# Kernel optimization log

Measured on AMD Instinct MI355X. Metric: run time of the kernel, lower is better.

Reference implementation:

```python
import jax, jax.numpy as jnp
import numpy as np

N_NODES = 32768
N_EDGES = 524288
NODE_DIM = 128
HIDDEN = 256
EDGE_DIM = 32


def setup_inputs() -> dict:
    key = jax.random.key(0)
    ks = jax.random.split(key, 12)
    s = 0.05
    return {
        "h": jax.random.normal(ks[0], (N_NODES, NODE_DIM), jnp.float32),
        "x": jax.random.normal(ks[1], (N_NODES, 3), jnp.float32) * 10.0,
        "edge_index": jax.random.randint(ks[2], (2, N_EDGES), 0, N_NODES, dtype=jnp.int32).astype(jnp.int64),
        "edge_dist": jax.random.uniform(ks[3], (N_EDGES,), jnp.float32) * 15.0,
        # edge_mlp: Linear(1, edge_dim) -> SiLU -> Linear(edge_dim, edge_dim)
        "We1": jax.random.normal(ks[4], (1, EDGE_DIM), jnp.float32) * s,
        "be1": jnp.zeros((EDGE_DIM,), jnp.float32),
        "We2": jax.random.normal(ks[5], (EDGE_DIM, EDGE_DIM), jnp.float32) * s,
        "be2": jnp.zeros((EDGE_DIM,), jnp.float32),
        # node_mlp: Linear(2*node+edge, hidden) -> SiLU -> Linear(hidden, node)
        "Wn1": jax.random.normal(ks[6], (2 * NODE_DIM + EDGE_DIM, HIDDEN), jnp.float32) * s,
        "bn1": jnp.zeros((HIDDEN,), jnp.float32),
        "Wn2": jax.random.normal(ks[7], (HIDDEN, NODE_DIM), jnp.float32) * s,
        "bn2": jnp.zeros((NODE_DIM,), jnp.float32),
        # coord_mlp: Linear(2*node+edge, hidden) -> SiLU -> Linear(hidden, 1, bias=False)
        "Wc1": jax.random.normal(ks[8], (2 * NODE_DIM + EDGE_DIM, HIDDEN), jnp.float32) * s,
        "bc1": jnp.zeros((HIDDEN,), jnp.float32),
        "Wc2": jax.random.normal(ks[9], (HIDDEN, 1), jnp.float32) * s,
    }


def reference(h, x, edge_index, edge_dist,
              We1, be1, We2, be2,
              Wn1, bn1, Wn2, bn2,
              Wc1, bc1, Wc2):
    src, dst = edge_index[0], edge_index[1]
    n_nodes = h.shape[0]

    # edge_mlp on scalar distances -> [E, edge_dim]
    edge_attr = jax.nn.silu(edge_dist[:, None] @ We1 + be1) @ We2 + be2

    # per-edge message input: [E, 2*node_dim + edge_dim]
    m_input = jnp.concatenate([h[src], h[dst], edge_attr], axis=-1)

    # node messages and scatter-add onto destination nodes
    m = jax.nn.silu(m_input @ Wn1 + bn1) @ Wn2 + bn2          # [E, node_dim]
    h_agg = jax.ops.segment_sum(m, dst, num_segments=n_nodes)  # [N, node_dim]

    # equivariant coordinate update along normalized edge direction
    coord_weight = jax.nn.silu(m_input @ Wc1 + bc1) @ Wc2      # [E, 1]
    dir_vec = x[src] - x[dst]                                  # [E, 3]
    dir_len = jnp.maximum(jnp.linalg.norm(dir_vec, axis=-1, keepdims=True), 1e-8)
    coord_update = coord_weight * (dir_vec / dir_len)          # [E, 3]
    x_agg = jax.ops.segment_sum(coord_update, dst, num_segments=n_nodes)

    return h + h_agg, x + x_agg
```

## Files before the change

### kernel.cpp

```cpp
#include <hip/hip_runtime.h>
#include <math.h>

#define N_NODES 32768
#define N_EDGES 524288
#define NODE_DIM 128
#define HIDDEN 256
#define EDGE_DIM 32
#define TE 32
#define NBLK (N_EDGES / TE)
#define ASTR 296
#define HSTR 264
#define SZ2  264
#define MSTR 132

typedef __attribute__((ext_vector_type(8))) short bf16x8;
typedef __attribute__((ext_vector_type(16))) float f32x16;

__device__ __forceinline__ float silu_f(float v) {
    float e = __expf(-v);
    return v * __builtin_amdgcn_rcpf(1.0f + e);
}

__device__ __forceinline__ unsigned short f2bf_rne(float f) {
    union { float f; unsigned int u; } v; v.f = f;
    return (unsigned short)((v.u + 0x7fffu + ((v.u >> 16) & 1u)) >> 16);
}
__device__ __forceinline__ unsigned int pk_rne(float a, float b) {
    return (unsigned int)f2bf_rne(a) | ((unsigned int)f2bf_rne(b) << 16);
}
__device__ __forceinline__ unsigned int pkbf(float a, float b) {
    union { float f; unsigned int u; } ua, ub; ua.f = a; ub.f = b;
    return __builtin_amdgcn_perm(ub.u + 0x8000u, ua.u + 0x8000u, 0x07060302u);
}
__device__ __forceinline__ unsigned short f2bf_hu(float f) {
    union { float f; unsigned int u; } v; v.f = f;
    return (unsigned short)((v.u + 0x8000u) >> 16);
}
__device__ __forceinline__ float bfu(unsigned short u) {
    union { unsigned int u; float f; } v; v.u = ((unsigned int)u) << 16;
    return v.f;
}
__device__ __forceinline__ unsigned int addbf2(unsigned int a, unsigned int b) {
    float l = __uint_as_float(a << 16) + __uint_as_float(b << 16);
    float h = __uint_as_float(a & 0xffff0000u) + __uint_as_float(b & 0xffff0000u);
    return pkbf(l, h);
}

__device__ __forceinline__ int detect_is64(const void* ei, int t) {
    const unsigned int* ew = (const unsigned int*)ei;
    unsigned int hiw = ew[2 * (t & 63) + 1];
    return (__ballot(hiw != 0u) == 0ULL) ? 1 : 0;
}

#define WS_BIAS_OFF 1024
#define WS_W1S_OFF  69632
#define WS_W2S_OFF  364544
#define WS_CNT_OFF  430080
#define WS_CUR_OFF  561152
#define WS_PERM_OFF 692224
#define WS_HBF_OFF  2790400
#define WS_HBF_END  (WS_HBF_OFF + N_NODES * NODE_DIM * 2)
#define WS_PS_OFF   WS_HBF_END
#define WS_PD_OFF   (WS_PS_OFF + N_NODES * 512 * 2)
#define WS_PD_END   (WS_PD_OFF + N_NODES * 512 * 2)

#define SEG_HIST 524288
#define SEG_W1S  147456
#define SEG_W2S  32768
#define SEG_BIAS 512
#define SEG_OUT  1073152
#define SEG_HBF  524288
#define PREP_TOT (SEG_HIST + SEG_W1S + SEG_W2S + SEG_BIAS + SEG_OUT + SEG_HBF)

#define W1_PA 0
#define W1_PB 16384
#define W1_PC 81920

__device__ __forceinline__ float w1row(const float* Wn1, const float* Wc1, int k, int n) {
    return (n < 256) ? Wn1[k * 256 + n] : Wc1[k * 256 + (n - 256)];
}

__global__ void prep_hist_kernel(const float* __restrict__ h, const float* __restrict__ x,
                                 const void* __restrict__ ei,
                                 const float* __restrict__ We2, const float* __restrict__ be2,
                                 const float* __restrict__ Wn1, const float* __restrict__ bn1,
                                 const float* __restrict__ Wn2,
                                 const float* __restrict__ Wc1, const float* __restrict__ bc1,
                                 float* __restrict__ out, float* __restrict__ biasC,
                                 unsigned short* __restrict__ W1s, unsigned short* __restrict__ W2s,
                                 int* __restrict__ counts, unsigned short* __restrict__ hbf,
                                 int use_pp) {
    int i = blockIdx.x * 256 + threadIdx.x;
    if (i < SEG_HIST) {
        int is64 = detect_is64(ei, threadIdx.x);
        int dst = is64 ? (int)((const long long*)ei)[N_EDGES + i]
                       : ((const int*)ei)[N_EDGES + i];
        atomicAdd(&counts[dst], 1);
        return;
    }
    i -= SEG_HIST;
    if (i < SEG_W1S) {
        if (use_pp) {
            if (i < W1_PB) {
                int jj = i & 7, ln = (i >> 3) & 63, rest = i >> 9;
                int step = rest & 1, tile = rest >> 1;
                int n = tile * 32 + (ln & 31);
                int j = step * 16 + ((ln >> 5) * 8) + jj;
                float s = 0.0f;
                #pragma unroll 8
                for (int q = 0; q < 32; ++q)
                    s += We2[j * 32 + q] * w1row(Wn1, Wc1, 256 + q, n);
                W1s[i] = f2bf_rne(s);
            } else if (i < W1_PC) {
                int i2 = i - W1_PB;
                int jj = i2 & 7, ln = (i2 >> 3) & 63, rest = i2 >> 9;
                int step = rest & 7, tile = rest >> 3;
                int n = tile * 32 + (ln & 31);
                int k = step * 16 + ((ln >> 5) * 8) + jj;
                W1s[i] = f2bf_rne(w1row(Wn1, Wc1, k, n));
            } else {
                int i2 = i - W1_PC;
                int jj = i2 & 7, ln = (i2 >> 3) & 63, rest = i2 >> 9;
                int step = rest & 7, tile = rest >> 3;
                int n = tile * 32 + (ln & 31);
                int k = 128 + step * 16 + ((ln >> 5) * 8) + jj;
                W1s[i] = f2bf_rne(w1row(Wn1, Wc1, k, n));
            }
        } else {
// ... 69 lines not shown
    int c = counts[b * 256 + t];
    loc[t] = c;
    __syncthreads();
    if (t == 0) {
        int s = 0;
        for (int j = 0; j < 128; ++j) { int v = pb[j]; pb[j] = s; s += v; }
    }
    #pragma unroll
    for (int d = 1; d < 256; d <<= 1) {
        int v = (t >= d) ? loc[t - d] : 0;
        __syncthreads();
        loc[t] += v;
        __syncthreads();
    }
    cursor[b * 256 + t] = pb[b] + loc[t] - c;
}

__global__ void place_kernel(const void* __restrict__ ei,
                             int* __restrict__ cursor, int* __restrict__ perm) {
    int is64 = detect_is64(ei, threadIdx.x);
    int e = blockIdx.x * 256 + threadIdx.x;
    int dst = is64 ? (int)((const long long*)ei)[N_EDGES + e]
                   : ((const int*)ei)[N_EDGES + e];
    int pos = atomicAdd(&cursor[dst], 1);
    perm[pos] = e;
}

__global__ __launch_bounds__(256, 4)
void nterm_kernel(const unsigned short* __restrict__ hbf,
                  const unsigned short* __restrict__ W1s,
                  unsigned short* __restrict__ psrc,
                  unsigned short* __restrict__ pdst) {
    const int t = threadIdx.x;
    const int lane = t & 63;
    const int wv = t >> 6;
    const int lo = lane & 31;
    const int hi = lane >> 5;
    const int nb = blockIdx.x * 32;
    const int aoff = (nb + lo) * NODE_DIM + hi * 8;
    const int TSB = 8 * 64 * 8;

    for (int pass = 0; pass < 2; ++pass) {
        const unsigned short* WB = W1s + (pass ? W1_PC : W1_PB);
        unsigned short* outp = pass ? pdst : psrc;
        f32x16 a0, a1, a2, a3;
        #pragma unroll
        for (int r = 0; r < 16; ++r) { a0[r] = 0.f; a1[r] = 0.f; a2[r] = 0.f; a3[r] = 0.f; }
        const int b0 = (wv     ) * TSB + lane * 8;
        const int b1 = (wv +  4) * TSB + lane * 8;
        const int b2 = (wv +  8) * TSB + lane * 8;
        const int b3 = (wv + 12) * TSB + lane * 8;
        bf16x8 p0[2], p1[2], p2[2], p3[2];
        p0[0] = *(const bf16x8*)&WB[b0];
        p1[0] = *(const bf16x8*)&WB[b1];
        p2[0] = *(const bf16x8*)&WB[b2];
        p3[0] = *(const bf16x8*)&WB[b3];
        #pragma unroll
        for (int step = 0; step < 8; ++step) {
            const int cur = step & 1, nxt = cur ^ 1;
            if (step + 1 < 8) {
                p0[nxt] = *(const bf16x8*)&WB[b0 + (step + 1) * 512];
                p1[nxt] = *(const bf16x8*)&WB[b1 + (step + 1) * 512];
                p2[nxt] = *(const bf16x8*)&WB[b2 + (step + 1) * 512];
                p3[nxt] = *(const bf16x8*)&WB[b3 + (step + 1) * 512];
            }
            bf16x8 f = *(const bf16x8*)&hbf[aoff + step * 16];
            a0 = __builtin_amdgcn_mfma_f32_32x32x16_bf16(f, p0[cur], a0, 0, 0, 0);
            a1 = __builtin_amdgcn_mfma_f32_32x32x16_bf16(f, p1[cur], a1, 0, 0, 0);
            a2 = __builtin_amdgcn_mfma_f32_32x32x16_bf16(f, p2[cur], a2, 0, 0, 0);
            a3 = __builtin_amdgcn_mfma_f32_32x32x16_bf16(f, p3[cur], a3, 0, 0, 0);
        }
        #pragma unroll
        for (int r = 0; r < 16; ++r) {
            int er = (r & 3) + 8 * (r >> 2) + 4 * hi;
            unsigned short* row = &outp[(unsigned)(nb + er) * 512 + lo];
            row[(wv     ) * 32] = f2bf_rne(a0[r]);
            row[(wv +  4) * 32] = f2bf_rne(a1[r]);
            row[(wv +  8) * 32] = f2bf_rne(a2[r]);
            row[(wv + 12) * 32] = f2bf_rne(a3[r]);
        }
    }
}

__global__ __launch_bounds__(256, 6)
void egnn_pp_kernel(const float* __restrict__ x,
                    const void* __restrict__ ei, const float* __restrict__ dist,
                    const float* __restrict__ We1, const float* __restrict__ be1,
                    const float* __restrict__ bn2, const float* __restrict__ Wc2,
                    const float* __restrict__ biasC,
                    const unsigned short* __restrict__ W1s,
                    const unsigned short* __restrict__ W2s,
                    const int* __restrict__ perm,
                    const unsigned short* __restrict__ psrc,
                    const unsigned short* __restrict__ pdst,
                    float* __restrict__ out)
{
    __shared__ unsigned short smZ[TE * SZ2];
    __shared__ unsigned short smT[TE * 40];
    __shared__ int sidx[TE], didx[TE], eidx[TE];
    __shared__ float cw_s[TE];
    __shared__ float cxyz[3 * TE];

    float* smM = (float*)smZ;

    const int t = threadIdx.x;
    const int lane = t & 63;
    const int wv = t >> 6;
    const int lo = lane & 31;
    const int hi = lane >> 5;
    const int swz = ((blockIdx.x & 7) * (NBLK / 8)) + (blockIdx.x >> 3);
    const int ebase = swz * TE;
    const int is64 = detect_is64(ei, t);

    if (t < 2 * TE) {
        int e = t & (TE - 1);
        int eid = perm[ebase + e];
        int which = t >> 5;
        long long pos = (long long)which * N_EDGES + eid;
        int idx = is64 ? (int)((const long long*)ei)[pos] : ((const int*)ei)[pos];
        if (which == 0) { sidx[e] = idx; eidx[e] = eid; }
        else didx[e] = idx;
        if (t < TE) cw_s[t] = 0.0f;
    }
    __syncthreads();

    {
        int e = t >> 3;
        int j4 = (t & 7) * 4;
        float d = dist[eidx[e]];
        float s0 = silu_f(d * We1[j4 + 0] + be1[j4 + 0]);
        float s1 = silu_f(d * We1[j4 + 1] + be1[j4 + 1]);
        float s2 = silu_f(d * We1[j4 + 2] + be1[j4 + 2]);
        float s3 = silu_f(d * We1[j4 + 3] + be1[j4 + 3]);
        *(uint2*)&smT[e * 40 + j4] = make_uint2(pkbf(s0, s1), pkbf(s2, s3));
    }
    if (t < TE) {
        int s = sidx[t], dn = didx[t];
        float dx = x[s * 3 + 0] - x[dn * 3 + 0];
        float dy = x[s * 3 + 1] - x[dn * 3 + 1];
        float dz = x[s * 3 + 2] - x[dn * 3 + 2];
        float len = fmaxf(sqrtf(dx * dx + dy * dy + dz * dz), 1e-8f);
        float inv = 1.0f / len;
        cxyz[t] = dx * inv; cxyz[TE + t] = dy * inv; cxyz[2 * TE + t] = dz * inv;
    }
    __syncthreads();

    const int rowbase = 4 * hi;
    const int aT = lo * 40 + hi * 8;

    #pragma unroll
    for (int it = 0; it < 4; ++it) {
        int id = it * 256 + t;
        int g = id & 31;
        int e = id >> 5;
        int cb = 256 + g * 8;
        uint4 a = *(const uint4*)&psrc[(unsigned)sidx[e] * 512 + cb];
        uint4 b = *(const uint4*)&pdst[(unsigned)didx[e] * 512 + cb];
        uint4 o = make_uint4(addbf2(a.x, b.x), addbf2(a.y, b.y),
                             addbf2(a.z, b.z), addbf2(a.w, b.w));
        *(uint4*)&smZ[e * SZ2 + g * 8] = o;
    }
    __syncthreads();

    {
        const int c0off = wv * 32;
        const int c1off = (wv + 4) * 32;
        f32x16 c0, c1;
        {
            float b0 = biasC[256 + c0off + lo];
            float b1 = biasC[256 + c1off + lo];
            #pragma unroll
            for (int r = 0; r < 16; ++r) { c0[r] = b0; c1[r] = b1; }
        }
        bf16x8 a0 = *(const bf16x8*)&smT[aT];
        bf16x8 a1 = *(const bf16x8*)&smT[aT + 16];
        const int tt0 = 8 + wv, tt1 = 12 + wv;
        bf16x8 w00 = *(const bf16x8*)&W1s[((tt0 * 2 + 0) * 64 + lane) * 8];
        bf16x8 w01 = *(const bf16x8*)&W1s[((tt0 * 2 + 1) * 64 + lane) * 8];
        bf16x8 w10 = *(const bf16x8*)&W1s[((tt1 * 2 + 0) * 64 + lane) * 8];
        bf16x8 w11 = *(const bf16x8*)&W1s[((tt1 * 2 + 1) * 64 + lane) * 8];
        c0 = __builtin_amdgcn_mfma_f32_32x32x16_bf16(a0, w00, c0, 0, 0, 0);
        c0 = __builtin_amdgcn_mfma_f32_32x32x16_bf16(a1, w01, c0, 0, 0, 0);
        c1 = __builtin_amdgcn_mfma_f32_32x32x16_bf16(a0, w10, c1, 0, 0, 0);
        c1 = __builtin_amdgcn_mfma_f32_32x32x16_bf16(a1, w11, c1, 0, 0, 0);
        float wc0 = Wc2[c0off + lo];
        float wc1 = Wc2[c1off + lo];
        float p[16];
        #pragma unroll
        for (int r = 0; r < 16; ++r) {
            int er = (r & 3) + 8 * (r >> 2) + rowbase;
            float v0 = c0[r] + bfu(smZ[er * SZ2 + c0off + lo]);
            float v1 = c1[r] + bfu(smZ[er * SZ2 + c1off + lo]);
            p[r] = silu_f(v0) * wc0 + silu_f(v1) * wc1;
        }
        #pragma unroll
        for (int off = 1; off < 32; off <<= 1) {
            #pragma unroll
            for (int r = 0; r < 16; ++r) p[r] += __shfl_xor(p[r], off);
        }
        if (lo == 0) {
            #pragma unroll
            for (int r = 0; r < 16; ++r)
                atomicAdd(&cw_s[(r & 3) + 8 * (r >> 2) + rowbase], p[r]);
        }
    }
    __syncthreads();

    #pragma unroll
    for (int it = 0; it < 4; ++it) {
        int id = it * 256 + t;
        int g = id & 31;
        int e = id >> 5;
        int cb = g * 8;
        uint4 a = *(const uint4*)&psrc[(unsigned)sidx[e] * 512 + cb];
        uint4 b = *(const uint4*)&pdst[(unsigned)didx[e] * 512 + cb];
        uint4 o = make_uint4(addbf2(a.x, b.x), addbf2(a.y, b.y),
                             addbf2(a.z, b.z), addbf2(a.w, b.w));
        *(uint4*)&smZ[e * SZ2 + g * 8] = o;
    }
    __syncthreads();

    {
        const int n0off = wv * 32;
        const int n1off = (wv + 4) * 32;
        f32x16 c0, c1;
        {
            float b0 = biasC[n0off + lo];
            float b1 = biasC[n1off + lo];
            #pragma unroll
            for (int r = 0; r < 16; ++r) { c0[r] = b0; c1[r] = b1; }
        }
        bf16x8 a0 = *(const bf16x8*)&smT[aT];
        bf16x8 a1 = *(const bf16x8*)&smT[aT + 16];
        const int tt0 = wv, tt1 = wv + 4;
        bf16x8 w00 = *(const bf16x8*)&W1s[((tt0 * 2 + 0) * 64 + lane) * 8];
        bf16x8 w01 = *(const bf16x8*)&W1s[((tt0 * 2 + 1) * 64 + lane) * 8];
        bf16x8 w10 = *(const bf16x8*)&W1s[((tt1 * 2 + 0) * 64 + lane) * 8];
        bf16x8 w11 = *(const bf16x8*)&W1s[((tt1 * 2 + 1) * 64 + lane) * 8];
        c0 = __builtin_amdgcn_mfma_f32_32x32x16_bf16(a0, w00, c0, 0, 0, 0);
        c0 = __builtin_amdgcn_mfma_f32_32x32x16_bf16(a1, w01, c0, 0, 0, 0);
        c1 = __builtin_amdgcn_mfma_f32_32x32x16_bf16(a0, w10, c1, 0, 0, 0);
        c1 = __builtin_amdgcn_mfma_f32_32x32x16_bf16(a1, w11, c1, 0, 0, 0);
        #pragma unroll
        for (int r = 0; r < 16; ++r) {
            int er = (r & 3) + 8 * (r >> 2) + rowbase;
            float v0 = c0[r] + bfu(smZ[er * SZ2 + n0off + lo]);
            float v1 = c1[r] + bfu(smZ[er * SZ2 + n1off + lo]);
            smZ[er * SZ2 + n0off + lo] = f2bf_hu(silu_f(v0));
            smZ[er * SZ2 + n1off + lo] = f2bf_hu(silu_f(v1));
        }
    }
    if (t < TE) {
        float w = cw_s[t];
        cxyz[t] *= w; cxyz[TE + t] *= w; cxyz[2 * TE + t] *= w;
    }
    __syncthreads();

    {
        const int d = wv * 32 + lo;
        f32x16 acc;
        float bb = bn2[d];
        #pragma unroll
        for (int r = 0; r < 16; ++r) acc[r] = bb;
        const int hoff = lo * SZ2 + hi * 8;
        const int wb = wv * (16 * 64 * 8) + lane * 8;
        bf16x8 bs[2];
        bs[0] = *(const bf16x8*)&W2s[wb];
        #pragma unroll
        for (int step = 0; step < 16; ++step) {
            const int cur = step & 1, nxt = cur ^ 1;
            if (step + 1 < 16)
                bs[nxt] = *(const bf16x8*)&W2s[wb + (step + 1) * 512];
            bf16x8 af = *(const bf16x8*)&smZ[hoff + step * 16];
            acc = __builtin_amdgcn_mfma_f32_32x32x16_bf16(af, bs[cur], acc, 0, 0, 0);
        }
        __syncthreads();
        #pragma unroll
        for (int r = 0; r < 16; ++r) {
            int er = (r & 3) + 8 * (r >> 2) + rowbase;
            smM[er * MSTR + d] = acc[r];
        }
    }
    __syncthreads();

    {
        const int g = t >> 5;
        const int d4 = (t & 31) * 4;
        for (int e0 = g; e0 < TE; e0 += 8) {
            if (e0 > 0 && didx[e0] == didx[e0 - 1]) continue;
            float4 s = *(const float4*)&smM[e0 * MSTR + d4];
            int er = e0 + 1;
            while (er < TE && didx[er] == didx[e0]) {
                float4 v = *(const float4*)&smM[er * MSTR + d4];
                s.x += v.x; s.y += v.y; s.z += v.z; s.w += v.w;
                ++er;
            }
            float* dp = &out[didx[e0] * NODE_DIM + d4];
            if (e0 > 0 && er < TE) {
                float4 cur = *(const float4*)dp;
                cur.x += s.x; cur.y += s.y; cur.z += s.z; cur.w += s.w;
                *(float4*)dp = cur;
            } else {
                atomicAdd(dp + 0, s.x); atomicAdd(dp + 1, s.y);
                atomicAdd(dp + 2, s.z); atomicAdd(dp + 3, s.w);
            }
        }
    }
    if (t < TE) {
        int e0 = t;
        if (e0 == 0 || didx[e0] != didx[e0 - 1]) {
            float sx = cxyz[e0], sy = cxyz[TE + e0], sz = cxyz[2 * TE + e0];
            int er = e0 + 1;
            while (er < TE && didx[er] == didx[e0]) {
                sx += cxyz[er]; sy += cxyz[TE + er]; sz += cxyz[2 * TE + er];
                ++er;
            }
            float* xo = out + N_NODES * NODE_DIM + didx[e0] * 3;
            if (e0 > 0 && er < TE) {
                xo[0] += sx; xo[1] += sy; xo[2] += sz;
            } else {
                atomicAdd(xo + 0, sx); atomicAdd(xo + 1, sy); atomicAdd(xo + 2, sz);
            }
        }
    }
}

__global__ __launch_bounds__(256, 6)
void egnn_mfma_kernel(const float* __restrict__ h, const float* __restrict__ x,
                      const void* __restrict__ ei, const float* __restrict__ dist,
                      const float* __restrict__ We1, const float* __restrict__ be1,
                      const float* __restrict__ bn2, const float* __restrict__ Wc2,
                      const float* __restrict__ biasC,
                      const unsigned short* __restrict__ W1s,
                      const unsigned short* __restrict__ W2s,
                      const int* __restrict__ perm,
                      const unsigned short* __restrict__ hbf,
                      float* __restrict__ out)
{
    __shared__ unsigned short smA[TE * ASTR];
    __shared__ int sidx[TE], didx[TE], eidx[TE];
    __shared__ float cw_s[TE];
    __shared__ float cxyz[3 * TE];

    unsigned short* smH = smA;
    float* smM = (float*)smA;

    const int t = threadIdx.x;
    const int lane = t & 63;
    const int wv = t >> 6;
    const int lo = lane & 31;
    const int hi = lane >> 5;
    const int swz = ((blockIdx.x & 7) * (NBLK / 8)) + (blockIdx.x >> 3);
    const int ebase = swz * TE;
    const int is64 = detect_is64(ei, t);

    if (t < 2 * TE) {
        int e = t & (TE - 1);
        int eid = perm[ebase + e];
        int which = t >> 5;
        long long pos = (long long)which * N_EDGES + eid;
        int idx = is64 ? (int)((const long long*)ei)[pos] : ((const int*)ei)[pos];
        if (which == 0) { sidx[e] = idx; eidx[e] = eid; }
        else didx[e] = idx;
        if (t < TE) cw_s[t] = 0.0f;
    }
    __syncthreads();

    if (hbf != nullptr) {
        #pragma unroll
        for (int it = 0; it < 4; ++it) {
            int id = it * 256 + t;
            int g = id & 15;
            int half = (id >> 4) & 1;
            int e = id >> 5;
            int node = half ? didx[e] : sidx[e];
            uint4 v = *(const uint4*)&hbf[node * NODE_DIM + 8 * g];
            *(uint4*)&smA[e * ASTR + half * NODE_DIM + 8 * g] = v;
        }
    } else {
        #pragma unroll
        for (int it = 0; it < 4; ++it) {
            int id = it * 256 + t;
            int g8 = id & 15;
            int half = (id >> 4) & 1;
            int e = id >> 5;
            int node = half ? didx[e] : sidx[e];
            const float4* p = (const float4*)&h[node * NODE_DIM + 8 * g8];
            float4 v0 = p[0], v1 = p[1];
            unsigned int a0 = pkbf(v0.x, v0.y), a1 = pkbf(v0.z, v0.w);
            unsigned int a2 = pkbf(v1.x, v1.y), a3 = pkbf(v1.z, v1.w);
            *(uint4*)&smA[e * ASTR + half * NODE_DIM + 8 * g8] = make_uint4(a0, a1, a2, a3);
        }
    }
    {
        int e = t >> 3;
        int j4 = (t & 7) * 4;
        float d = dist[eidx[e]];
        float s0 = silu_f(d * We1[j4 + 0] + be1[j4 + 0]);
        float s1 = silu_f(d * We1[j4 + 1] + be1[j4 + 1]);
        float s2 = silu_f(d * We1[j4 + 2] + be1[j4 + 2]);
        float s3 = silu_f(d * We1[j4 + 3] + be1[j4 + 3]);
        *(uint2*)&smA[e * ASTR + 2 * NODE_DIM + j4] = make_uint2(pkbf(s0, s1), pkbf(s2, s3));
    }
    if (t < TE) {
        int s = sidx[t], dn = didx[t];
        float dx = x[s * 3 + 0] - x[dn * 3 + 0];
        float dy = x[s * 3 + 1] - x[dn * 3 + 1];
        float dz = x[s * 3 + 2] - x[dn * 3 + 2];
        float len = fmaxf(sqrtf(dx * dx + dy * dy + dz * dz), 1e-8f);
        float inv = 1.0f / len;
        cxyz[t] = dx * inv; cxyz[TE + t] = dy * inv; cxyz[2 * TE + t] = dz * inv;
    }
    __syncthreads();

    const int rowbase = 4 * hi;

    {
        f32x16 c0, c1;
        {
            float b0 = biasC[256 + wv * 32 + lo];
            float b1 = biasC[256 + (wv + 4) * 32 + lo];
            #pragma unroll
            for (int r = 0; r < 16; ++r) { c0[r] = b0; c1[r] = b1; }
        }
        {
            const int ao = lo * ASTR + hi * 8;
            const int TS = 18 * 64 * 8;
            const int q0 = (8 + wv) * TS + lane * 8;
            const int q1 = (12 + wv) * TS + lane * 8;
            bf16x8 p0[2], p1[2];
            p0[0] = *(const bf16x8*)&W1s[q0];
            p1[0] = *(const bf16x8*)&W1s[q1];
            #pragma unroll
            for (int step = 0; step < 18; ++step) {
                const int cur = step & 1, nxt = cur ^ 1;
                if (step + 1 < 18) {
                    p0[nxt] = *(const bf16x8*)&W1s[q0 + (step + 1) * 512];
                    p1[nxt] = *(const bf16x8*)&W1s[q1 + (step + 1) * 512];
                }
                bf16x8 f = *(const bf16x8*)&smA[ao + step * 16];
                c0 = __builtin_amdgcn_mfma_f32_32x32x16_bf16(f, p0[cur], c0, 0, 0, 0);
                c1 = __builtin_amdgcn_mfma_f32_32x32x16_bf16(f, p1[cur], c1, 0, 0, 0);
            }
        }
        float w0 = Wc2[wv * 32 + lo];
        float w1 = Wc2[(wv + 4) * 32 + lo];
        float p[16];
        #pragma unroll
        for (int r = 0; r < 16; ++r)
            p[r] = silu_f(c0[r]) * w0 + silu_f(c1[r]) * w1;
        #pragma unroll
        for (int off = 1; off < 32; off <<= 1) {
            #pragma unroll
            for (int r = 0; r < 16; ++r) p[r] += __shfl_xor(p[r], off);
        }
        if (lo == 0) {
            #pragma unroll
            for (int r = 0; r < 16; ++r)
                atomicAdd(&cw_s[(r & 3) + 8 * (r >> 2) + rowbase], p[r]);
        }
    }

    f32x16 a0, a1;
    {
        float b0 = biasC[wv * 32 + lo];
        float b1 = biasC[(wv + 4) * 32 + lo];
        #pragma unroll
        for (int r = 0; r < 16; ++r) { a0[r] = b0; a1[r] = b1; }
        const int ao = lo * ASTR + hi * 8;
        const int TS = 18 * 64 * 8;
        const int q0 = (wv) * TS + lane * 8;
        const int q1 = (wv + 4) * TS + lane * 8;
        bf16x8 p0[2], p1[2];
        p0[0] = *(const bf16x8*)&W1s[q0];
        p1[0] = *(const bf16x8*)&W1s[q1];
        #pragma unroll
        for (int step = 0; step < 18; ++step) {
            const int cur = step & 1, nxt = cur ^ 1;
            if (step + 1 < 18) {
                p0[nxt] = *(const bf16x8*)&W1s[q0 + (step + 1) * 512];
                p1[nxt] = *(const bf16x8*)&W1s[q1 + (step + 1) * 512];
            }
            bf16x8 f = *(const bf16x8*)&smA[ao + step * 16];
            a0 = __builtin_amdgcn_mfma_f32_32x32x16_bf16(f, p0[cur], a0, 0, 0, 0);
            a1 = __builtin_amdgcn_mfma_f32_32x32x16_bf16(f, p1[cur], a1, 0, 0, 0);
        }
    }
    __syncthreads();

    {
        const int jb0 = (wv    ) * 32 + lo;
        const int jb1 = (wv + 4) * 32 + lo;
        #pragma unroll
        for (int r = 0; r < 16; ++r) {
            int er = (r & 3) + 8 * (r >> 2) + rowbase;
            smH[er * HSTR + jb0] = f2bf_hu(silu_f(a0[r]));
            smH[er * HSTR + jb1] = f2bf_hu(silu_f(a1[r]));
        }
    }
    if (t < TE) {
        float w = cw_s[t];
        cxyz[t] *= w; cxyz[TE + t] *= w; cxyz[2 * TE + t] *= w;
    }
    __syncthreads();

    {
        const int d = wv * 32 + lo;
        f32x16 acc;
        float bb = bn2[d];
        #pragma unroll
        for (int r = 0; r < 16; ++r) acc[r] = bb;
        const int hoff = lo * HSTR + hi * 8;
        const int wb = wv * (16 * 64 * 8) + lane * 8;
        bf16x8 bs[2];
        bs[0] = *(const bf16x8*)&W2s[wb];
        #pragma unroll
        for (int step = 0; step < 16; ++step) {
            const int cur = step & 1, nxt = cur ^ 1;
            if (step + 1 < 16)
                bs[nxt] = *(const bf16x8*)&W2s[wb + (step + 1) * 512];
            bf16x8 af = *(const bf16x8*)&smH[hoff + step * 16];
            acc = __builtin_amdgcn_mfma_f32_32x32x16_bf16(af, bs[cur], acc, 0, 0, 0);
        }
        __syncthreads();
        #pragma unroll
        for (int r = 0; r < 16; ++r) {
            int er = (r & 3) + 8 * (r >> 2) + rowbase;
            smM[er * MSTR + d] = acc[r];
        }
    }
    __syncthreads();

    {
        const int g = t >> 5;
        const int d4 = (t & 31) * 4;
        for (int e0 = g; e0 < TE; e0 += 8) {
            if (e0 > 0 && didx[e0] == didx[e0 - 1]) continue;
            float4 s = *(const float4*)&smM[e0 * MSTR + d4];
            int er = e0 + 1;
            while (er < TE && didx[er] == didx[e0]) {
                float4 v = *(const float4*)&smM[er * MSTR + d4];
                s.x += v.x; s.y += v.y; s.z += v.z; s.w += v.w;
                ++er;
            }
            float* dp = &out[didx[e0] * NODE_DIM + d4];
            if (e0 > 0 && er < TE) {
                float4 cur = *(const float4*)dp;
                cur.x += s.x; cur.y += s.y; cur.z += s.z; cur.w += s.w;
                *(float4*)dp = cur;
            } else {
                atomicAdd(dp + 0, s.x); atomicAdd(dp + 1, s.y);
                atomicAdd(dp + 2, s.z); atomicAdd(dp + 3, s.w);
            }
        }
    }
    if (t < TE) {
        int e0 = t;
        if (e0 == 0 || didx[e0] != didx[e0 - 1]) {
            float sx = cxyz[e0], sy = cxyz[TE + e0], sz = cxyz[2 * TE + e0];
            int er = e0 + 1;
            while (er < TE && didx[er] == didx[e0]) {
                sx += cxyz[er]; sy += cxyz[TE + er]; sz += cxyz[2 * TE + er];
                ++er;
            }
            float* xo = out + N_NODES * NODE_DIM + didx[e0] * 3;
            if (e0 > 0 && er < TE) {
                xo[0] += sx; xo[1] += sy; xo[2] += sz;
            } else {
                atomicAdd(xo + 0, sx); atomicAdd(xo + 1, sy); atomicAdd(xo + 2, sz);
            }
        }
    }
}

extern "C" void kernel_launch(void* const* d_in, const int* in_sizes, int n_in,
                              void* d_out, int out_size, void* d_ws, size_t ws_size,
                              hipStream_t stream) {
    const float* h    = (const float*)d_in[0];
    const float* x    = (const float*)d_in[1];
    const void*  ei   = d_in[2];
    const float* dist = (const float*)d_in[3];
    const float* We1  = (const float*)d_in[4];
    const float* be1  = (const float*)d_in[5];
    const float* We2  = (const float*)d_in[6];
    const float* be2  = (const float*)d_in[7];
    const float* Wn1  = (const float*)d_in[8];
    const float* bn1  = (const float*)d_in[9];
    const float* Wn2  = (const float*)d_in[10];
    const float* bn2  = (const float*)d_in[11];
    const float* Wc1  = (const float*)d_in[12];
    const float* bc1  = (const float*)d_in[13];
    const float* Wc2  = (const float*)d_in[14];
    float* out = (float*)d_out;

    float* biasC = (float*)((char*)d_ws + WS_BIAS_OFF);
    unsigned short* W1s = (unsigned short*)((char*)d_ws + WS_W1S_OFF);
    unsigned short* W2s = (unsigned short*)((char*)d_ws + WS_W2S_OFF);
    int* counts   = (int*)((char*)d_ws + WS_CNT_OFF);
    int* cursor   = (int*)((char*)d_ws + WS_CUR_OFF);
    int* perm     = (int*)((char*)d_ws + WS_PERM_OFF);
    unsigned short* hbf = (ws_size >= (size_t)WS_HBF_END)
                        ? (unsigned short*)((char*)d_ws + WS_HBF_OFF) : nullptr;
    int use_pp = (ws_size >= (size_t)WS_PD_END && hbf != nullptr) ? 1 : 0;
    unsigned short* psrc = use_pp ? (unsigned short*)((char*)d_ws + WS_PS_OFF) : nullptr;
    unsigned short* pdst = use_pp ? (unsigned short*)((char*)d_ws + WS_PD_OFF) : nullptr;
// ... 20 lines not shown
```

Measured before the change: 404.5 us.

## Add gathered src/dst projections via identity-matrix MFMAs instead of LDS staging

The precomputed per-node projections (psrc, pdst) used to be gathered, summed in bf16 and staged through shared memory before the edge-feature MFMAs. Each lane now loads its rows straight from global memory and adds them into the accumulators with extra MFMAs against identity bf16 matrices. This removes the LDS staging stores, the bf16 add and two block barriers, at the cost of eight extra MFMAs per half and more live registers. The occupancy hint is lowered from 6 to 5 waves to make room for those registers.

```diff
diff --git a/kernel.cpp b/kernel.cpp
--- a/kernel.cpp
+++ b/kernel.cpp
@@ -39,11 +39,6 @@
 __device__ __forceinline__ float bfu(unsigned short u) {
     union { unsigned int u; float f; } v; v.u = ((unsigned int)u) << 16;
     return v.f;
-}
-__device__ __forceinline__ unsigned int addbf2(unsigned int a, unsigned int b) {
-    float l = __uint_as_float(a << 16) + __uint_as_float(b << 16);
-    float h = __uint_as_float(a & 0xffff0000u) + __uint_as_float(b & 0xffff0000u);
-    return pkbf(l, h);
 }
 
 __device__ __forceinline__ int detect_is64(const void* ei, int t) {
@@ -279,7 +274,7 @@
     }
 }
 
-__global__ __launch_bounds__(256, 6)
+__global__ __launch_bounds__(256, 5)
 void egnn_pp_kernel(const float* __restrict__ x,
                     const void* __restrict__ ei, const float* __restrict__ dist,
                     const float* __restrict__ We1, const float* __restrict__ be1,
@@ -292,13 +287,13 @@
                     const unsigned short* __restrict__ pdst,
                     float* __restrict__ out)
 {
-    __shared__ unsigned short smZ[TE * SZ2];
+    __shared__ unsigned short smH[TE * SZ2];
     __shared__ unsigned short smT[TE * 40];
     __shared__ int sidx[TE], didx[TE], eidx[TE];
     __shared__ float cw_s[TE];
     __shared__ float cxyz[3 * TE];
 
-    float* smM = (float*)smZ;
+    float* smM = (float*)smH;
 
     const int t = threadIdx.x;
     const int lane = t & 63;
@@ -345,23 +340,31 @@
     const int rowbase = 4 * hi;
     const int aT = lo * 40 + hi * 8;
 
+    bf16x8 ilow, ihigh;
     #pragma unroll
-    for (int it = 0; it < 4; ++it) {
-        int id = it * 256 + t;
-        int g = id & 31;
-        int e = id >> 5;
-        int cb = 256 + g * 8;
-        uint4 a = *(const uint4*)&psrc[(unsigned)sidx[e] * 512 + cb];
-        uint4 b = *(const uint4*)&pdst[(unsigned)didx[e] * 512 + cb];
-        uint4 o = make_uint4(addbf2(a.x, b.x), addbf2(a.y, b.y),
-                             addbf2(a.z, b.z), addbf2(a.w, b.w));
-        *(uint4*)&smZ[e * SZ2 + g * 8] = o;
-    }
-    __syncthreads();
+    for (int idx = 0; idx < 8; ++idx) {
+        int k = hi * 8 + idx;
+        ilow[idx]  = (short)((k == lo)      ? 0x3F80 : 0);
+        ihigh[idx] = (short)((k == lo - 16) ? 0x3F80 : 0);
+    }
+
+    const unsigned int bs = (unsigned)sidx[lo] * 512 + hi * 8;
+    const unsigned int bd = (unsigned)didx[lo] * 512 + hi * 8;
+
+    bf16x8 a0 = *(const bf16x8*)&smT[aT];
+    bf16x8 a1 = *(const bf16x8*)&smT[aT + 16];
 
     {
         const int c0off = wv * 32;
         const int c1off = (wv + 4) * 32;
+        bf16x8 zs00 = *(const bf16x8*)&psrc[bs + 256 + c0off];
+        bf16x8 zs01 = *(const bf16x8*)&psrc[bs + 256 + c0off + 16];
+        bf16x8 zd00 = *(const bf16x8*)&pdst[bd + 256 + c0off];
+        bf16x8 zd01 = *(const bf16x8*)&pdst[bd + 256 + c0off + 16];
+        bf16x8 zs10 = *(const bf16x8*)&psrc[bs + 256 + c1off];
+        bf16x8 zs11 = *(const bf16x8*)&psrc[bs + 256 + c1off + 16];
+        bf16x8 zd10 = *(const bf16x8*)&pdst[bd + 256 + c1off];
+        bf16x8 zd11 = *(const bf16x8*)&pdst[bd + 256 + c1off + 16];
         f32x16 c0, c1;
         {
             float b0 = biasC[256 + c0off + lo];
@@ -369,8 +372,6 @@
             #pragma unroll
             for (int r = 0; r < 16; ++r) { c0[r] = b0; c1[r] = b1; }
         }
-        bf16x8 a0 = *(const bf16x8*)&smT[aT];
-        bf16x8 a1 = *(const bf16x8*)&smT[aT + 16];
         const int tt0 = 8 + wv, tt1 = 12 + wv;
         bf16x8 w00 = *(const bf16x8*)&W1s[((tt0 * 2 + 0) * 64 + lane) * 8];
         bf16x8 w01 = *(const bf16x8*)&W1s[((tt0 * 2 + 1) * 64 + lane) * 8];
@@ -380,16 +381,20 @@
         c0 = __builtin_amdgcn_mfma_f32_32x32x16_bf16(a1, w01, c0, 0, 0, 0);
         c1 = __builtin_amdgcn_mfma_f32_32x32x16_bf16(a0, w10, c1, 0, 0, 0);
         c1 = __builtin_amdgcn_mfma_f32_32x32x16_bf16(a1, w11, c1, 0, 0, 0);
+        c0 = __builtin_amdgcn_mfma_f32_32x32x16_bf16(zs00, ilow,  c0, 0, 0, 0);
+        c0 = __builtin_amdgcn_mfma_f32_32x32x16_bf16(zs01, ihigh, c0, 0, 0, 0);
+        c0 = __builtin_amdgcn_mfma_f32_32x32x16_bf16(zd00, ilow,  c0, 0, 0, 0);
+        c0 = __builtin_amdgcn_mfma_f32_32x32x16_bf16(zd01, ihigh, c0, 0, 0, 0);
+        c1 = __builtin_amdgcn_mfma_f32_32x32x16_bf16(zs10, ilow,  c1, 0, 0, 0);
+        c1 = __builtin_amdgcn_mfma_f32_32x32x16_bf16(zs11, ihigh, c1, 0, 0, 0);
+        c1 = __builtin_amdgcn_mfma_f32_32x32x16_bf16(zd10, ilow,  c1, 0, 0, 0);
+        c1 = __builtin_amdgcn_mfma_f32_32x32x16_bf16(zd11, ihigh, c1, 0, 0, 0);
         float wc0 = Wc2[c0off + lo];
         float wc1 = Wc2[c1off + lo];
         float p[16];
         #pragma unroll
-        for (int r = 0; r < 16; ++r) {
-            int er = (r & 3) + 8 * (r >> 2) + rowbase;
-            float v0 = c0[r] + bfu(smZ[er * SZ2 + c0off + lo]);
-            float v1 = c1[r] + bfu(smZ[er * SZ2 + c1off + lo]);
-            p[r] = silu_f(v0) * wc0 + silu_f(v1) * wc1;
-        }
+        for (int r = 0; r < 16; ++r)
+            p[r] = silu_f(c0[r]) * wc0 + silu_f(c1[r]) * wc1;
         #pragma unroll
         for (int off = 1; off < 32; off <<= 1) {
             #pragma unroll
@@ -401,25 +406,18 @@
                 atomicAdd(&cw_s[(r & 3) + 8 * (r >> 2) + rowbase], p[r]);
         }
     }
-    __syncthreads();
-
-    #pragma unroll
-    for (int it = 0; it < 4; ++it) {
-        int id = it * 256 + t;
-        int g = id & 31;
-        int e = id >> 5;
-        int cb = g * 8;
-        uint4 a = *(const uint4*)&psrc[(unsigned)sidx[e] * 512 + cb];
-        uint4 b = *(const uint4*)&pdst[(unsigned)didx[e] * 512 + cb];
-        uint4 o = make_uint4(addbf2(a.x, b.x), addbf2(a.y, b.y),
-                             addbf2(a.z, b.z), addbf2(a.w, b.w));
-        *(uint4*)&smZ[e * SZ2 + g * 8] = o;
-    }
-    __syncthreads();
 
     {
         const int n0off = wv * 32;
         const int n1off = (wv + 4) * 32;
+        bf16x8 zs00 = *(const bf16x8*)&psrc[bs + n0off];
+        bf16x8 zs01 = *(const bf16x8*)&psrc[bs + n0off + 16];
+        bf16x8 zd00 = *(const bf16x8*)&pdst[bd + n0off];
+        bf16x8 zd01 = *(const bf16x8*)&pdst[bd + n0off + 16];
+        bf16x8 zs10 = *(const bf16x8*)&psrc[bs + n1off];
+        bf16x8 zs11 = *(const bf16x8*)&psrc[bs + n1off + 16];
+        bf16x8 zd10 = *(const bf16x8*)&pdst[bd + n1off];
+        bf16x8 zd11 = *(const bf16x8*)&pdst[bd + n1off + 16];
         f32x16 c0, c1;
         {
             float b0 = biasC[n0off + lo];
@@ -427,8 +425,6 @@
             #pragma unroll
             for (int r = 0; r < 16; ++r) { c0[r] = b0; c1[r] = b1; }
         }
-        bf16x8 a0 = *(const bf16x8*)&smT[aT];
-        bf16x8 a1 = *(const bf16x8*)&smT[aT + 16];
         const int tt0 = wv, tt1 = wv + 4;
         bf16x8 w00 = *(const bf16x8*)&W1s[((tt0 * 2 + 0) * 64 + lane) * 8];
         bf16x8 w01 = *(const bf16x8*)&W1s[((tt0 * 2 + 1) * 64 + lane) * 8];
@@ -438,20 +434,27 @@
         c0 = __builtin_amdgcn_mfma_f32_32x32x16_bf16(a1, w01, c0, 0, 0, 0);
         c1 = __builtin_amdgcn_mfma_f32_32x32x16_bf16(a0, w10, c1, 0, 0, 0);
         c1 = __builtin_amdgcn_mfma_f32_32x32x16_bf16(a1, w11, c1, 0, 0, 0);
+        c0 = __builtin_amdgcn_mfma_f32_32x32x16_bf16(zs00, ilow,  c0, 0, 0, 0);
+        c0 = __builtin_amdgcn_mfma_f32_32x32x16_bf16(zs01, ihigh, c0, 0, 0, 0);
+        c0 = __builtin_amdgcn_mfma_f32_32x32x16_bf16(zd00, ilow,  c0, 0, 0, 0);
+        c0 = __builtin_amdgcn_mfma_f32_32x32x16_bf16(zd01, ihigh, c0, 0, 0, 0);
+        c1 = __builtin_amdgcn_mfma_f32_32x32x16_bf16(zs10, ilow,  c1, 0, 0, 0);
+        c1 = __builtin_amdgcn_mfma_f32_32x32x16_bf16(zs11, ihigh, c1, 0, 0, 0);
+        c1 = __builtin_amdgcn_mfma_f32_32x32x16_bf16(zd10, ilow,  c1, 0, 0, 0);
+        c1 = __builtin_amdgcn_mfma_f32_32x32x16_bf16(zd11, ihigh, c1, 0, 0, 0);
         #pragma unroll
         for (int r = 0; r < 16; ++r) {
             int er = (r & 3) + 8 * (r >> 2) + rowbase;
-            float v0 = c0[r] + bfu(smZ[er * SZ2 + n0off + lo]);
-            float v1 = c1[r] + bfu(smZ[er * SZ2 + n1off + lo]);
-            smZ[er * SZ2 + n0off + lo] = f2bf_hu(silu_f(v0));
-            smZ[er * SZ2 + n1off + lo] = f2bf_hu(silu_f(v1));
-        }
-    }
+            smH[er * SZ2 + n0off + lo] = f2bf_hu(silu_f(c0[r]));
+            smH[er * SZ2 + n1off + lo] = f2bf_hu(silu_f(c1[r]));
+        }
+    }
+    __syncthreads();
+
     if (t < TE) {
         float w = cw_s[t];
         cxyz[t] *= w; cxyz[TE + t] *= w; cxyz[2 * TE + t] *= w;
     }
-    __syncthreads();
 
     {
         const int d = wv * 32 + lo;
@@ -461,15 +464,15 @@
         for (int r = 0; r < 16; ++r) acc[r] = bb;
         const int hoff = lo * SZ2 + hi * 8;
         const int wb = wv * (16 * 64 * 8) + lane * 8;
-        bf16x8 bs[2];
-        bs[0] = *(const bf16x8*)&W2s[wb];
+        bf16x8 bs2[2];
+        bs2[0] = *(const bf16x8*)&W2s[wb];
         #pragma unroll
         for (int step = 0; step < 16; ++step) {
             const int cur = step & 1, nxt = cur ^ 1;
             if (step + 1 < 16)
-                bs[nxt] = *(const bf16x8*)&W2s[wb + (step + 1) * 512];
-            bf16x8 af = *(const bf16x8*)&smZ[hoff + step * 16];
-            acc = __builtin_amdgcn_mfma_f32_32x32x16_bf16(af, bs[cur], acc, 0, 0, 0);
+                bs2[nxt] = *(const bf16x8*)&W2s[wb + (step + 1) * 512];
+            bf16x8 af = *(const bf16x8*)&smH[hoff + step * 16];
+            acc = __builtin_amdgcn_mfma_f32_32x32x16_bf16(af, bs2[cur], acc, 0, 0, 0);
         }
         __syncthreads();
         #pragma unroll
@@ -539,7 +542,7 @@
     __shared__ float cw_s[TE];
     __shared__ float cxyz[3 * TE];
 
-    unsigned short* smH = smA;
+    unsigned short* smH2 = smA;
     float* smM = (float*)smA;
 
     const int t = threadIdx.x;
@@ -691,8 +694,8 @@
         #pragma unroll
         for (int r = 0; r < 16; ++r) {
             int er = (r & 3) + 8 * (r >> 2) + rowbase;
-            smH[er * HSTR + jb0] = f2bf_hu(silu_f(a0[r]));
-            smH[er * HSTR + jb1] = f2bf_hu(silu_f(a1[r]));
+            smH2[er * HSTR + jb0] = f2bf_hu(silu_f(a0[r]));
+            smH2[er * HSTR + jb1] = f2bf_hu(silu_f(a1[r]));
         }
     }
     if (t < TE) {
@@ -709,15 +712,15 @@
         for (int r = 0; r < 16; ++r) acc[r] = bb;
         const int hoff = lo * HSTR + hi * 8;
         const int wb = wv * (16 * 64 * 8) + lane * 8;
-        bf16x8 bs[2];
-        bs[0] = *(const bf16x8*)&W2s[wb];
+        bf16x8 bs2[2];
+        bs2[0] = *(const bf16x8*)&W2s[wb];
         #pragma unroll
         for (int step = 0; step < 16; ++step) {
             const int cur = step & 1, nxt = cur ^ 1;
             if (step + 1 < 16)
-                bs[nxt] = *(const bf16x8*)&W2s[wb + (step + 1) * 512];
-            bf16x8 af = *(const bf16x8*)&smH[hoff + step * 16];
-            acc = __builtin_amdgcn_mfma_f32_32x32x16_bf16(af, bs[cur], acc, 0, 0, 0);
+                bs2[nxt] = *(const bf16x8*)&W2s[wb + (step + 1) * 512];
+            bf16x8 af = *(const bf16x8*)&smH2[hoff + step * 16];
+            acc = __builtin_amdgcn_mfma_f32_32x32x16_bf16(af, bs2[cur], acc, 0, 0, 0);
         }
         __syncthreads();
         #pragma unroll
```

Result: slower. 422.3 us (+4.4%).

## Accumulate gathered src/dst projections into MFMA accumulators via identity matmuls

Applied to the files above, without the earlier changes.

Instead of adding the gathered bf16 source and destination projections elementwise into shared memory, the edge kernel loads each projection into LDS separately. It then adds it to the accumulator tiles with MFMA against identity bf16 matrices, so the bias, edge-feature and gather contributions all sum in fp32 registers. This drops the scalar bf16 add/unpack work and the per-element LDS reads in the epilogue. In exchange it needs twice as many gather passes and barriers plus extra MFMAs and registers, so the occupancy hint is lowered from 6 to 5 waves.

```diff
diff --git a/kernel.cpp b/kernel.cpp
--- a/kernel.cpp
+++ b/kernel.cpp
@@ -39,11 +39,6 @@
 __device__ __forceinline__ float bfu(unsigned short u) {
     union { unsigned int u; float f; } v; v.u = ((unsigned int)u) << 16;
     return v.f;
-}
-__device__ __forceinline__ unsigned int addbf2(unsigned int a, unsigned int b) {
-    float l = __uint_as_float(a << 16) + __uint_as_float(b << 16);
-    float h = __uint_as_float(a & 0xffff0000u) + __uint_as_float(b & 0xffff0000u);
-    return pkbf(l, h);
 }
 
 __device__ __forceinline__ int detect_is64(const void* ei, int t) {
@@ -279,7 +274,7 @@
     }
 }
 
-__global__ __launch_bounds__(256, 6)
+__global__ __launch_bounds__(256, 5)
 void egnn_pp_kernel(const float* __restrict__ x,
                     const void* __restrict__ ei, const float* __restrict__ dist,
                     const float* __restrict__ We1, const float* __restrict__ be1,
@@ -298,6 +293,7 @@
     __shared__ float cw_s[TE];
     __shared__ float cxyz[3 * TE];
 
+    unsigned short* smH = smZ;
     float* smM = (float*)smZ;
 
     const int t = threadIdx.x;
@@ -340,66 +336,56 @@
         float inv = 1.0f / len;
         cxyz[t] = dx * inv; cxyz[TE + t] = dy * inv; cxyz[2 * TE + t] = dz * inv;
     }
-    __syncthreads();
-
-    const int rowbase = 4 * hi;
-    const int aT = lo * 40 + hi * 8;
-
     #pragma unroll
     for (int it = 0; it < 4; ++it) {
         int id = it * 256 + t;
         int g = id & 31;
         int e = id >> 5;
-        int cb = 256 + g * 8;
-        uint4 a = *(const uint4*)&psrc[(unsigned)sidx[e] * 512 + cb];
-        uint4 b = *(const uint4*)&pdst[(unsigned)didx[e] * 512 + cb];
-        uint4 o = make_uint4(addbf2(a.x, b.x), addbf2(a.y, b.y),
-                             addbf2(a.z, b.z), addbf2(a.w, b.w));
-        *(uint4*)&smZ[e * SZ2 + g * 8] = o;
-    }
-    __syncthreads();
-
-    {
-        const int c0off = wv * 32;
-        const int c1off = (wv + 4) * 32;
-        f32x16 c0, c1;
-        {
-            float b0 = biasC[256 + c0off + lo];
-            float b1 = biasC[256 + c1off + lo];
-            #pragma unroll
-            for (int r = 0; r < 16; ++r) { c0[r] = b0; c1[r] = b1; }
-        }
-        bf16x8 a0 = *(const bf16x8*)&smT[aT];
-        bf16x8 a1 = *(const bf16x8*)&smT[aT + 16];
+        uint4 v = *(const uint4*)&psrc[(unsigned)sidx[e] * 512 + 256 + g * 8];
+        *(uint4*)&smZ[e * SZ2 + g * 8] = v;
+    }
+    __syncthreads();
+
+    const int rowbase = 4 * hi;
+    const int aT = lo * 40 + hi * 8;
+    const int zb = lo * SZ2 + hi * 8;
+
+    bf16x8 ilow, ihigh;
+    #pragma unroll
+    for (int ii = 0; ii < 8; ++ii) {
+        int k = hi * 8 + ii;
+        ilow[ii]  = (short)((k == lo)      ? 0x3F80 : 0);
+        ihigh[ii] = (short)((k == lo - 16) ? 0x3F80 : 0);
+    }
+
+    bf16x8 a0T = *(const bf16x8*)&smT[aT];
+    bf16x8 a1T = *(const bf16x8*)&smT[aT + 16];
+
+    f32x16 c0, c1;
+    {
+        float b0 = biasC[256 + wv * 32 + lo];
+        float b1 = biasC[256 + (wv + 4) * 32 + lo];
+        #pragma unroll
+        for (int r = 0; r < 16; ++r) { c0[r] = b0; c1[r] = b1; }
+    }
+    {
         const int tt0 = 8 + wv, tt1 = 12 + wv;
         bf16x8 w00 = *(const bf16x8*)&W1s[((tt0 * 2 + 0) * 64 + lane) * 8];
         bf16x8 w01 = *(const bf16x8*)&W1s[((tt0 * 2 + 1) * 64 + lane) * 8];
         bf16x8 w10 = *(const bf16x8*)&W1s[((tt1 * 2 + 0) * 64 + lane) * 8];
         bf16x8 w11 = *(const bf16x8*)&W1s[((tt1 * 2 + 1) * 64 + lane) * 8];
-        c0 = __builtin_amdgcn_mfma_f32_32x32x16_bf16(a0, w00, c0, 0, 0, 0);
-        c0 = __builtin_amdgcn_mfma_f32_32x32x16_bf16(a1, w01, c0, 0, 0, 0);
-        c1 = __builtin_amdgcn_mfma_f32_32x32x16_bf16(a0, w10, c1, 0, 0, 0);
-        c1 = __builtin_amdgcn_mfma_f32_32x32x16_bf16(a1, w11, c1, 0, 0, 0);
-        float wc0 = Wc2[c0off + lo];
-        float wc1 = Wc2[c1off + lo];
-        float p[16];
-        #pragma unroll
-        for (int r = 0; r < 16; ++r) {
-            int er = (r & 3) + 8 * (r >> 2) + rowbase;
-            float v0 = c0[r] + bfu(smZ[er * SZ2 + c0off + lo]);
-            float v1 = c1[r] + bfu(smZ[er * SZ2 + c1off + lo]);
-            p[r] = silu_f(v0) * wc0 + silu_f(v1) * wc1;
-        }
-        #pragma unroll
-        for (int off = 1; off < 32; off <<= 1) {
-            #pragma unroll
-            for (int r = 0; r < 16; ++r) p[r] += __shfl_xor(p[r], off);
-        }
-        if (lo == 0) {
-            #pragma unroll
-            for (int r = 0; r < 16; ++r)
-                atomicAdd(&cw_s[(r & 3) + 8 * (r >> 2) + rowbase], p[r]);
-        }
+        c0 = __builtin_amdgcn_mfma_f32_32x32x16_bf16(a0T, w00, c0, 0, 0, 0);
+        c0 = __builtin_amdgcn_mfma_f32_32x32x16_bf16(a1T, w01, c0, 0, 0, 0);
+        c1 = __builtin_amdgcn_mfma_f32_32x32x16_bf16(a0T, w10, c1, 0, 0, 0);
+        c1 = __builtin_amdgcn_mfma_f32_32x32x16_bf16(a1T, w11, c1, 0, 0, 0);
+        bf16x8 z00 = *(const bf16x8*)&smZ[zb + wv * 32];
+        bf16x8 z01 = *(const bf16x8*)&smZ[zb + wv * 32 + 16];
+        bf16x8 z10 = *(const bf16x8*)&smZ[zb + (wv + 4) * 32];
+        bf16x8 z11 = *(const bf16x8*)&smZ[zb + (wv + 4) * 32 + 16];
+        c0 = __builtin_amdgcn_mfma_f32_32x32x16_bf16(z00, ilow,  c0, 0, 0, 0);
+        c0 = __builtin_amdgcn_mfma_f32_32x32x16_bf16(z01, ihigh, c0, 0, 0, 0);
+        c1 = __builtin_amdgcn_mfma_f32_32x32x16_bf16(z10, ilow,  c1, 0, 0, 0);
+        c1 = __builtin_amdgcn_mfma_f32_32x32x16_bf16(z11, ihigh, c1, 0, 0, 0);
     }
     __syncthreads();
 
@@ -408,44 +394,94 @@
         int id = it * 256 + t;
         int g = id & 31;
         int e = id >> 5;
-        int cb = g * 8;
-        uint4 a = *(const uint4*)&psrc[(unsigned)sidx[e] * 512 + cb];
-        uint4 b = *(const uint4*)&pdst[(unsigned)didx[e] * 512 + cb];
-        uint4 o = make_uint4(addbf2(a.x, b.x), addbf2(a.y, b.y),
-                             addbf2(a.z, b.z), addbf2(a.w, b.w));
-        *(uint4*)&smZ[e * SZ2 + g * 8] = o;
-    }
-    __syncthreads();
-
-    {
-        const int n0off = wv * 32;
-        const int n1off = (wv + 4) * 32;
-        f32x16 c0, c1;
-        {
-            float b0 = biasC[n0off + lo];
-            float b1 = biasC[n1off + lo];
+        uint4 v = *(const uint4*)&pdst[(unsigned)didx[e] * 512 + 256 + g * 8];
+        *(uint4*)&smZ[e * SZ2 + g * 8] = v;
+    }
+    __syncthreads();
+
+    {
+        bf16x8 z00 = *(const bf16x8*)&smZ[zb + wv * 32];
+        bf16x8 z01 = *(const bf16x8*)&smZ[zb + wv * 32 + 16];
+        bf16x8 z10 = *(const bf16x8*)&smZ[zb + (wv + 4) * 32];
+        bf16x8 z11 = *(const bf16x8*)&smZ[zb + (wv + 4) * 32 + 16];
+        c0 = __builtin_amdgcn_mfma_f32_32x32x16_bf16(z00, ilow,  c0, 0, 0, 0);
+        c0 = __builtin_amdgcn_mfma_f32_32x32x16_bf16(z01, ihigh, c0, 0, 0, 0);
+        c1 = __builtin_amdgcn_mfma_f32_32x32x16_bf16(z10, ilow,  c1, 0, 0, 0);
+        c1 = __builtin_amdgcn_mfma_f32_32x32x16_bf16(z11, ihigh, c1, 0, 0, 0);
+        float wc0 = Wc2[wv * 32 + lo];
+        float wc1 = Wc2[(wv + 4) * 32 + lo];
+        float p[16];
+        #pragma unroll
+        for (int r = 0; r < 16; ++r)
+            p[r] = silu_f(c0[r]) * wc0 + silu_f(c1[r]) * wc1;
+        #pragma unroll
+        for (int off = 1; off < 32; off <<= 1) {
             #pragma unroll
-            for (int r = 0; r < 16; ++r) { c0[r] = b0; c1[r] = b1; }
-        }
-        bf16x8 a0 = *(const bf16x8*)&smT[aT];
-        bf16x8 a1 = *(const bf16x8*)&smT[aT + 16];
+            for (int r = 0; r < 16; ++r) p[r] += __shfl_xor(p[r], off);
+        }
+        if (lo == 0) {
+            #pragma unroll
+            for (int r = 0; r < 16; ++r)
+                atomicAdd(&cw_s[(r & 3) + 8 * (r >> 2) + rowbase], p[r]);
+        }
+    }
+    __syncthreads();
+
+    #pragma unroll
+    for (int it = 0; it < 4; ++it) {
+        int id = it * 256 + t;
+        int g = id & 31;
+        int e = id >> 5;
+        uint4 v = *(const uint4*)&psrc[(unsigned)sidx[e] * 512 + g * 8];
+        *(uint4*)&smZ[e * SZ2 + g * 8] = v;
+    }
+    __syncthreads();
+
+    f32x16 n0, n1;
+    {
+        float b0 = biasC[wv * 32 + lo];
+        float b1 = biasC[(wv + 4) * 32 + lo];
+        #pragma unroll
+        for (int r = 0; r < 16; ++r) { n0[r] = b0; n1[r] = b1; }
         const int tt0 = wv, tt1 = wv + 4;
         bf16x8 w00 = *(const bf16x8*)&W1s[((tt0 * 2 + 0) * 64 + lane) * 8];
         bf16x8 w01 = *(const bf16x8*)&W1s[((tt0 * 2 + 1) * 64 + lane) * 8];
         bf16x8 w10 = *(const bf16x8*)&W1s[((tt1 * 2 + 0) * 64 + lane) * 8];
         bf16x8 w11 = *(const bf16x8*)&W1s[((tt1 * 2 + 1) * 64 + lane) * 8];
-        c0 = __builtin_amdgcn_mfma_f32_32x32x16_bf16(a0, w00, c0, 0, 0, 0);
-        c0 = __builtin_amdgcn_mfma_f32_32x32x16_bf16(a1, w01, c0, 0, 0, 0);
-        c1 = __builtin_amdgcn_mfma_f32_32x32x16_bf16(a0, w10, c1, 0, 0, 0);
-        c1 = __builtin_amdgcn_mfma_f32_32x32x16_bf16(a1, w11, c1, 0, 0, 0);
-        #pragma unroll
-        for (int r = 0; r < 16; ++r) {
-            int er = (r & 3) + 8 * (r >> 2) + rowbase;
-            float v0 = c0[r] + bfu(smZ[er * SZ2 + n0off + lo]);
-            float v1 = c1[r] + bfu(smZ[er * SZ2 + n1off + lo]);
-            smZ[er * SZ2 + n0off + lo] = f2bf_hu(silu_f(v0));
-            smZ[er * SZ2 + n1off + lo] = f2bf_hu(silu_f(v1));
-        }
+        n0 = __builtin_amdgcn_mfma_f32_32x32x16_bf16(a0T, w00, n0, 0, 0, 0);
+        n0 = __builtin_amdgcn_mfma_f32_32x32x16_bf16(a1T, w01, n0, 0, 0, 0);
+        n1 = __builtin_amdgcn_mfma_f32_32x32x16_bf16(a0T, w10, n1, 0, 0, 0);
+        n1 = __builtin_amdgcn_mfma_f32_32x32x16_bf16(a1T, w11, n1, 0, 0, 0);
+        bf16x8 z00 = *(const bf16x8*)&smZ[zb + wv * 32];
+        bf16x8 z01 = *(const bf16x8*)&smZ[zb + wv * 32 + 16];
+        bf16x8 z10 = *(const bf16x8*)&smZ[zb + (wv + 4) * 32];
+        bf16x8 z11 = *(const bf16x8*)&smZ[zb + (wv + 4) * 32 + 16];
+        n0 = __builtin_amdgcn_mfma_f32_32x32x16_bf16(z00, ilow,  n0, 0, 0, 0);
+        n0 = __builtin_amdgcn_mfma_f32_32x32x16_bf16(z01, ihigh, n0, 0, 0, 0);
+        n1 = __builtin_amdgcn_mfma_f32_32x32x16_bf16(z10, ilow,  n1, 0, 0, 0);
+        n1 = __builtin_amdgcn_mfma_f32_32x32x16_bf16(z11, ihigh, n1, 0, 0, 0);
+    }
+    __syncthreads();
+
+    #pragma unroll
+    for (int it = 0; it < 4; ++it) {
+        int id = it * 256 + t;
+        int g = id & 31;
+        int e = id >> 5;
+        uint4 v = *(const uint4*)&pdst[(unsigned)didx[e] * 512 + g * 8];
+        *(uint4*)&smZ[e * SZ2 + g * 8] = v;
+    }
+    __syncthreads();
+
+    {
+        bf16x8 z00 = *(const bf16x8*)&smZ[zb + wv * 32];
+        bf16x8 z01 = *(const bf16x8*)&smZ[zb + wv * 32 + 16];
+        bf16x8 z10 = *(const bf16x8*)&smZ[zb + (wv + 4) * 32];
+        bf16x8 z11 = *(const bf16x8*)&smZ[zb + (wv + 4) * 32 + 16];
+        n0 = __builtin_amdgcn_mfma_f32_32x32x16_bf16(z00, ilow,  n0, 0, 0, 0);
+        n0 = __builtin_amdgcn_mfma_f32_32x32x16_bf16(z01, ihigh, n0, 0, 0, 0);
+        n1 = __builtin_amdgcn_mfma_f32_32x32x16_bf16(z10, ilow,  n1, 0, 0, 0);
+        n1 = __builtin_amdgcn_mfma_f32_32x32x16_bf16(z11, ihigh, n1, 0, 0, 0);
     }
     if (t < TE) {
         float w = cw_s[t];
@@ -453,6 +489,14 @@
     }
     __syncthreads();
 
+    #pragma unroll
+    for (int r = 0; r < 16; ++r) {
+        int er = (r & 3) + 8 * (r >> 2) + rowbase;
+        smH[er * SZ2 + wv * 32 + lo]       = f2bf_hu(silu_f(n0[r]));
+        smH[er * SZ2 + (wv + 4) * 32 + lo] = f2bf_hu(silu_f(n1[r]));
+    }
+    __syncthreads();
+
     {
         const int d = wv * 32 + lo;
         f32x16 acc;
@@ -461,15 +505,15 @@
         for (int r = 0; r < 16; ++r) acc[r] = bb;
         const int hoff = lo * SZ2 + hi * 8;
         const int wb = wv * (16 * 64 * 8) + lane * 8;
-        bf16x8 bs[2];
-        bs[0] = *(const bf16x8*)&W2s[wb];
+        bf16x8 bs2[2];
+        bs2[0] = *(const bf16x8*)&W2s[wb];
         #pragma unroll
         for (int step = 0; step < 16; ++step) {
             const int cur = step & 1, nxt = cur ^ 1;
             if (step + 1 < 16)
-                bs[nxt] = *(const bf16x8*)&W2s[wb + (step + 1) * 512];
-            bf16x8 af = *(const bf16x8*)&smZ[hoff + step * 16];
-            acc = __builtin_amdgcn_mfma_f32_32x32x16_bf16(af, bs[cur], acc, 0, 0, 0);
+                bs2[nxt] = *(const bf16x8*)&W2s[wb + (step + 1) * 512];
+            bf16x8 af = *(const bf16x8*)&smH[hoff + step * 16];
+            acc = __builtin_amdgcn_mfma_f32_32x32x16_bf16(af, bs2[cur], acc, 0, 0, 0);
         }
         __syncthreads();
         #pragma unroll
@@ -539,7 +583,7 @@
     __shared__ float cw_s[TE];
     __shared__ float cxyz[3 * TE];
 
-    unsigned short* smH = smA;
+    unsigned short* smH2 = smA;
     float* smM = (float*)smA;
 
     const int t = threadIdx.x;
@@ -691,8 +735,8 @@
         #pragma unroll
         for (int r = 0; r < 16; ++r) {
             int er = (r & 3) + 8 * (r >> 2) + rowbase;
-            smH[er * HSTR + jb0] = f2bf_hu(silu_f(a0[r]));
-            smH[er * HSTR + jb1] = f2bf_hu(silu_f(a1[r]));
+            smH2[er * HSTR + jb0] = f2bf_hu(silu_f(a0[r]));
+            smH2[er * HSTR + jb1] = f2bf_hu(silu_f(a1[r]));
         }
     }
     if (t < TE) {
@@ -709,15 +753,15 @@
         for (int r = 0; r < 16; ++r) acc[r] = bb;
         const int hoff = lo * HSTR + hi * 8;
         const int wb = wv * (16 * 64 * 8) + lane * 8;
-        bf16x8 bs[2];
-        bs[0] = *(const bf16x8*)&W2s[wb];
+        bf16x8 bs2[2];
+        bs2[0] = *(const bf16x8*)&W2s[wb];
         #pragma unroll
         for (int step = 0; step < 16; ++step) {
             const int cur = step & 1, nxt = cur ^ 1;
             if (step + 1 < 16)
-                bs[nxt] = *(const bf16x8*)&W2s[wb + (step + 1) * 512];
-            bf16x8 af = *(const bf16x8*)&smH[hoff + step * 16];
-            acc = __builtin_amdgcn_mfma_f32_32x32x16_bf16(af, bs[cur], acc, 0, 0, 0);
+                bs2[nxt] = *(const bf16x8*)&W2s[wb + (step + 1) * 512];
+            bf16x8 af = *(const bf16x8*)&smH2[hoff + step * 16];
+            acc = __builtin_amdgcn_mfma_f32_32x32x16_bf16(af, bs2[cur], acc, 0, 0, 0);
         }
         __syncthreads();
         #pragma unroll
```

Result: slower. 420.8 us (+4.0%).
